# Kernel optimization log

Measured on AMD Instinct MI355X. Metric: run time of the kernel, lower is better.

## Reference

```python
import jax, jax.numpy as jnp
import numpy as np

EPS = 1e-6  # matches module eps


def _l2_norm_ch(t):
    # normalize over channel axis (dim=-2), matching torch l2_norm helper
    return t / jnp.linalg.norm(t, axis=-2, keepdims=True)


def setup_inputs() -> dict:
    key = jax.random.key(0)
    ks = jax.random.split(key, 8)
    B, C, H, W = 8, 256, 128, 128
    m = C // 2  # scale=2
    x = jax.random.normal(ks[0], (B, C, H, W), dtype=jnp.float32)
    Wq = jax.random.normal(ks[1], (m, C), dtype=jnp.float32) * 0.05
    bq = jax.random.normal(ks[2], (m,), dtype=jnp.float32) * 0.05
    Wk = jax.random.normal(ks[3], (m, C), dtype=jnp.float32) * 0.05
    bk = jax.random.normal(ks[4], (m,), dtype=jnp.float32) * 0.05
    Wv = jax.random.normal(ks[5], (C, C), dtype=jnp.float32) * 0.05
    bv = jax.random.normal(ks[6], (C,), dtype=jnp.float32) * 0.05
    # gamma is a zero-init nn.Parameter in the module; use a random scalar so
    # the output is non-trivial for correctness checking.
    gamma = jax.random.normal(ks[7], (1,), dtype=jnp.float32)
    return {"x": x, "Wq": Wq, "bq": bq, "Wk": Wk, "bk": bk, "Wv": Wv, "bv": bv, "gamma": gamma}


def reference(x, Wq, bq, Wk, bk, Wv, bv, gamma):
    B, C, H, W = x.shape  # module names these (batch, channels, width, height)
    N = H * W
    xf = x.reshape(B, C, N)
    # 1x1 convs == per-pixel linear maps over channels
    Q = jnp.einsum('mc,bcn->bmn', Wq, xf) + bq[None, :, None]   # [B, m, N]
    K = jnp.einsum('mc,bcn->bmn', Wk, xf) + bk[None, :, None]   # [B, m, N]
    V = jnp.einsum('oc,bcn->bon', Wv, xf) + bv[None, :, None]   # [B, C, N]
    Qn = _l2_norm_ch(Q).transpose(0, 2, 1)  # [B, N, m]
    Kn = _l2_norm_ch(K)                      # [B, m, N]
    Ksum = jnp.sum(Kn, axis=-1) + EPS        # [B, m]
    tailor = 1.0 / (N + jnp.einsum('bnm,bm->bn', Qn, Ksum))  # [B, N]
    vsum = jnp.sum(V, axis=-1)                                # [B, C]
    matrix = jnp.einsum('bmn,bcn->bmc', Kn, V)                # [B, m, C]
    matrix_sum = vsum[:, :, None] + jnp.einsum('bnm,bmc->bcn', Qn, matrix)  # [B, C, N]
    weight_value = matrix_sum * tailor[:, None, :]
    return (gamma * weight_value).reshape(B, C, H, W)
```

## Files before the change

### kernel.cpp

```cpp
#include <hip/hip_runtime.h>
#include <math.h>

typedef unsigned short ushort_t;
typedef __attribute__((ext_vector_type(4))) float f32x4;
typedef __attribute__((ext_vector_type(8))) short short8;

#define MFMA16(a, b, c) __builtin_amdgcn_mfma_f32_16x16x32_bf16((a), (b), (c), 0, 0, 0)

constexpr int kB = 8;
constexpr int kC = 256;
constexpr int kM = 128;
constexpr int kN = 16384;

constexpr size_t kOffS    = 0;
constexpr size_t kOffKsum = 1048576;
constexpr size_t kOffXsum = 1052672;
constexpr size_t kOffVsum = 1060864;
constexpr size_t kOffWkb  = 1069056;
constexpr size_t kOffWqb  = 1134592;
constexpr size_t kOffMatT = 1200128;

__device__ __forceinline__ ushort_t f2bf(float f) {
  union { float f; unsigned u; } v; v.f = f;
  unsigned r = v.u + 0x7fffu + ((v.u >> 16) & 1u);
  return (ushort_t)(r >> 16);
}
__device__ __forceinline__ float bf2f(ushort_t h) {
  union { float f; unsigned u; } v; v.u = ((unsigned)h) << 16;
  return v.f;
}

__device__ __forceinline__ void sync_lds() {
  __atomic_signal_fence(__ATOMIC_SEQ_CST);
  __builtin_amdgcn_s_waitcnt(0xc07f);
  __builtin_amdgcn_s_barrier();
  __atomic_signal_fence(__ATOMIC_SEQ_CST);
}

__global__ void k0_init(const float* __restrict__ Wq, const float* __restrict__ Wk,
                        float* __restrict__ ws_f, ushort_t* __restrict__ Wkb,
                        ushort_t* __restrict__ Wqb) {
  int i = blockIdx.x * 256 + threadIdx.x;
  for (int j = i; j < 265216; j += 262144) ws_f[j] = 0.0f;
  if (i < kM * kC) {
    Wkb[i] = f2bf(Wk[i]);
    Wqb[i] = f2bf(Wq[i]);
  }
}

__global__ __launch_bounds__(512, 2)
void k1_acc(const float* __restrict__ x, const float* __restrict__ bk,
            const ushort_t* __restrict__ Wkb, float* __restrict__ S,
            float* __restrict__ Ksum, float* __restrict__ xsum) {
  __shared__ __align__(16) ushort_t xb_n[256][40];
  __shared__ __align__(16) ushort_t xb_t[32][264];
  __shared__ __align__(16) ushort_t knb[128][40];
  __shared__ __align__(16) float red[32][12];

  const int t = threadIdx.x;
  const int b = blockIdx.y;
  const int lane = t & 63, w = t >> 6, quad = lane >> 4, l16 = lane & 15;
  const int r8 = t >> 3;
  const int px0 = 4 * (t & 7);

  float bk_r[4];
#pragma unroll
  for (int r = 0; r < 4; ++r) bk_r[r] = bk[16 * w + 4 * quad + r];

  f32x4 accS[16];
#pragma unroll
  for (int ct = 0; ct < 16; ++ct) accS[ct] = (f32x4){0.f, 0.f, 0.f, 0.f};
  float ksump[4] = {0.f, 0.f, 0.f, 0.f};
  float xs_p[4] = {0.f, 0.f, 0.f, 0.f};

  const float* xg = x + ((size_t)(b * kC) + r8) * kN + blockIdx.x * 256 + px0;

  float4 bufA[4], bufB[4];
#pragma unroll
  for (int p = 0; p < 4; ++p)
    bufA[p] = *(const float4*)(xg + (size_t)p * 64 * kN);

  auto step = [&](int ti, float4 (&cur)[4], float4 (&nxt)[4]) {
    sync_lds();
    if (ti < 7) {
#pragma unroll
      for (int p = 0; p < 4; ++p)
        nxt[p] = *(const float4*)(xg + (size_t)p * 64 * kN + (ti + 1) * 32);
    }
#pragma unroll
    for (int p = 0; p < 4; ++p) {
      float4 v = cur[p];
      const int rp = 64 * p + r8;
      xs_p[p] += v.x + v.y + v.z + v.w;
      ushort_t u0 = f2bf(v.x), u1 = f2bf(v.y), u2 = f2bf(v.z), u3 = f2bf(v.w);
      uint2 pk;
      pk.x = (unsigned)u0 | ((unsigned)u1 << 16);
      pk.y = (unsigned)u2 | ((unsigned)u3 << 16);
      *(uint2*)&xb_n[rp][px0] = pk;
      xb_t[px0 + 0][rp] = u0;
      xb_t[px0 + 1][rp] = u1;
      xb_t[px0 + 2][rp] = u2;
      xb_t[px0 + 3][rp] = u3;
    }
    sync_lds();

    f32x4 acc1[2] = {{0.f, 0.f, 0.f, 0.f}, {0.f, 0.f, 0.f, 0.f}};
    const ushort_t* wkbase = Wkb + (16 * w + l16) * 256 + quad * 8;
#pragma unroll
    for (int ks = 0; ks < 8; ++ks) {
      short8 a = *(const short8*)(wkbase + ks * 32);
      short8 b0 = *(const short8*)&xb_t[l16][ks * 32 + quad * 8];
      short8 b1 = *(const short8*)&xb_t[16 + l16][ks * 32 + quad * 8];
      acc1[0] = MFMA16(a, b0, acc1[0]);
      acc1[1] = MFMA16(a, b1, acc1[1]);
    }
    float k0v[4], k1v[4];
    float ssq0 = 0.f, ssq1 = 0.f;
#pragma unroll
    for (int r = 0; r < 4; ++r) {
      k0v[r] = acc1[0][r] + bk_r[r];
      k1v[r] = acc1[1][r] + bk_r[r];
      ssq0 += k0v[r] * k0v[r];
      ssq1 += k1v[r] * k1v[r];
    }
    ssq0 += __shfl_xor(ssq0, 16); ssq0 += __shfl_xor(ssq0, 32);
    ssq1 += __shfl_xor(ssq1, 16); ssq1 += __shfl_xor(ssq1, 32);
    if (quad == 0) { red[l16][w] = ssq0; red[16 + l16][w] = ssq1; }
    sync_lds();

    f32x4 ra = *(const f32x4*)&red[l16][0];
    f32x4 rb = *(const f32x4*)&red[l16][4];
    f32x4 rc = *(const f32x4*)&red[16 + l16][0];
    f32x4 rd = *(const f32x4*)&red[16 + l16][4];
    const float iv0 = rsqrtf(ra[0] + ra[1] + ra[2] + ra[3] + rb[0] + rb[1] + rb[2] + rb[3]);
    const float iv1 = rsqrtf(rc[0] + rc[1] + rc[2] + rc[3] + rd[0] + rd[1] + rd[2] + rd[3]);
#pragma unroll
    for (int r = 0; r < 4; ++r) {
      float kn0 = k0v[r] * iv0, kn1 = k1v[r] * iv1;
      ksump[r] += kn0 + kn1;
      knb[16 * w + 4 * quad + r][l16] = f2bf(kn0);
      knb[16 * w + 4 * quad + r][16 + l16] = f2bf(kn1);
    }
    __builtin_amdgcn_s_waitcnt(0xc07f);

    short8 a2 = *(const short8*)&knb[16 * w + l16][quad * 8];
#pragma unroll
    for (int ct = 0; ct < 16; ++ct) {
      short8 b2 = *(const short8*)&xb_n[ct * 16 + l16][quad * 8];
      accS[ct] = MFMA16(a2, b2, accS[ct]);
    }
  };

  for (int ti = 0; ti < 8; ti += 2) {
    step(ti, bufA, bufB);
    step(ti + 1, bufB, bufA);
  }

  float* Sb = S + (size_t)b * kM * kC;
#pragma unroll
  for (int ct = 0; ct < 16; ++ct)
#pragma unroll
    for (int r = 0; r < 4; ++r)
      atomicAdd(&Sb[(16 * w + 4 * quad + r) * 256 + ct * 16 + l16], accS[ct][r]);
#pragma unroll
  for (int r = 0; r < 4; ++r) {
    float v = ksump[r];
    v += __shfl_xor(v, 1); v += __shfl_xor(v, 2);
    v += __shfl_xor(v, 4); v += __shfl_xor(v, 8);
    if (l16 == 0) atomicAdd(&Ksum[b * kM + 16 * w + 4 * quad + r], v);
  }
#pragma unroll
  for (int p = 0; p < 4; ++p) {
    float v = xs_p[p];
    v += __shfl_xor(v, 1); v += __shfl_xor(v, 2); v += __shfl_xor(v, 4);
    if ((t & 7) == 0) atomicAdd(&xsum[b * kC + 64 * p + r8], v);
  }
}

__global__ __launch_bounds__(256, 4)
void k2_matrix(const float* __restrict__ S, const float* __restrict__ Ksum,
               const float* __restrict__ xsum, const float* __restrict__ Wv,
               const float* __restrict__ bv, ushort_t* __restrict__ matT,
               float* __restrict__ vsum) {
  const int t = threadIdx.x;
  const int lane = t & 63, w = t >> 6, quad = lane >> 4, l16 = lane & 15;
  const int bx = blockIdx.x;
  const int b = bx >> 5, ct = (bx >> 1) & 15, mt = bx & 1;
  const int c0 = ct * 16;
  const int m0 = mt * 64 + w * 16;

  const float* arow = Wv + (size_t)(c0 + l16) * 256 + quad * 8;
  const float* brow = S + ((size_t)b * kM + m0 + l16) * 256 + quad * 8;
  const bool do_vsum = (mt == 0) && (w == 0);
  const float* xsb = xsum + b * kC + quad * 8;

  f32x4 acc = (f32x4){0.f, 0.f, 0.f, 0.f};
  float vdot = 0.f;

#pragma unroll
  for (int ks = 0; ks < 8; ++ks) {
    float4 a0 = *(const float4*)(arow + ks * 32);
    float4 a1 = *(const float4*)(arow + ks * 32 + 4);
    float4 b0 = *(const float4*)(brow + ks * 32);
    float4 b1 = *(const float4*)(brow + ks * 32 + 4);
    float av[8] = {a0.x, a0.y, a0.z, a0.w, a1.x, a1.y, a1.z, a1.w};
    float bw[8] = {b0.x, b0.y, b0.z, b0.w, b1.x, b1.y, b1.z, b1.w};
    if (do_vsum) {
      float4 x0 = *(const float4*)(xsb + ks * 32);
      float4 x1 = *(const float4*)(xsb + ks * 32 + 4);
      vdot += av[0] * x0.x + av[1] * x0.y + av[2] * x0.z + av[3] * x0.w +
              av[4] * x1.x + av[5] * x1.y + av[6] * x1.z + av[7] * x1.w;
    }
    short8 ah, al, bh, bl;
#pragma unroll
    for (int i = 0; i < 8; ++i) {
      ushort_t h = f2bf(av[i]);
      ah[i] = (short)h;
      al[i] = (short)f2bf(av[i] - bf2f(h));
      ushort_t g = f2bf(bw[i]);
      bh[i] = (short)g;
      bl[i] = (short)f2bf(bw[i] - bf2f(g));
    }
    acc = MFMA16(ah, bh, acc);
    acc = MFMA16(ah, bl, acc);
    acc = MFMA16(al, bh, acc);
  }

  const float ksm = Ksum[b * kM + m0 + l16];
  float4 bv4 = *(const float4*)(bv + c0 + quad * 4);
  float bvv[4] = {bv4.x, bv4.y, bv4.z, bv4.w};
#pragma unroll
  for (int r = 0; r < 4; ++r) {
    const int c = c0 + 4 * quad + r;
    matT[((size_t)b * kC + c) * kM + m0 + l16] = f2bf(acc[r] + ksm * bvv[r]);
  }
  if (do_vsum) {
    vdot += __shfl_xor(vdot, 16);
    vdot += __shfl_xor(vdot, 32);
    if (quad == 0)
      vsum[b * kC + c0 + l16] = vdot + 16384.f * bv[c0 + l16];
  }
}

__global__ __launch_bounds__(512, 2)
void k3_out(const float* __restrict__ x, const float* __restrict__ bq,
            const ushort_t* __restrict__ Wqb, const ushort_t* __restrict__ matT,
            const float* __restrict__ Ksum, const float* __restrict__ vsum,
            const float* __restrict__ gamma, float* __restrict__ out) {
  __shared__ __align__(16) ushort_t xb_t[32][264];
  __shared__ __align__(16) ushort_t qnb[32][136];
  __shared__ __align__(16) float red[32][12];
  __shared__ __align__(16) float red2[32][12];

  const int t = threadIdx.x;
  const int b = blockIdx.y;
  const int lane = t & 63, w = t >> 6, quad = lane >> 4, l16 = lane & 15;
  const int r8 = t >> 3;
  const int px0 = 4 * (t & 7);
  const float gm = gamma[0];

  float bq_r[4], ks_r[4], vs_r[2][4];
#pragma unroll
  for (int r = 0; r < 4; ++r) {
    bq_r[r] = bq[16 * w + 4 * quad + r];
    ks_r[r] = Ksum[b * kM + 16 * w + 4 * quad + r] + 1e-6f;
  }
#pragma unroll
  for (int mi = 0; mi < 2; ++mi)
#pragma unroll
    for (int r = 0; r < 4; ++r)
      vs_r[mi][r] = vsum[b * kC + (2 * w + mi) * 16 + 4 * quad + r];

  const float* xg = x + ((size_t)(b * kC) + r8) * kN + blockIdx.x * 256 + px0;

  float4 bufA[4], bufB[4];
#pragma unroll
  for (int p = 0; p < 4; ++p)
    bufA[p] = *(const float4*)(xg + (size_t)p * 64 * kN);

  auto step = [&](int ti, float4 (&cur)[4], float4 (&nxt)[4]) {
    const int n0 = blockIdx.x * 256 + ti * 32;
    sync_lds();
    if (ti < 7) {
#pragma unroll
      for (int p = 0; p < 4; ++p)
        nxt[p] = *(const float4*)(xg + (size_t)p * 64 * kN + (ti + 1) * 32);
    }
#pragma unroll
    for (int p = 0; p < 4; ++p) {
      float4 v = cur[p];
      const int rp = 64 * p + r8;
      xb_t[px0 + 0][rp] = f2bf(v.x);
      xb_t[px0 + 1][rp] = f2bf(v.y);
      xb_t[px0 + 2][rp] = f2bf(v.z);
      xb_t[px0 + 3][rp] = f2bf(v.w);
    }
    sync_lds();

    f32x4 acc1[2] = {{0.f, 0.f, 0.f, 0.f}, {0.f, 0.f, 0.f, 0.f}};
    const ushort_t* wqbase = Wqb + (16 * w + l16) * 256 + quad * 8;
#pragma unroll
    for (int ks = 0; ks < 8; ++ks) {
      short8 a = *(const short8*)(wqbase + ks * 32);
      short8 b0 = *(const short8*)&xb_t[l16][ks * 32 + quad * 8];
      short8 b1 = *(const short8*)&xb_t[16 + l16][ks * 32 + quad * 8];
      acc1[0] = MFMA16(a, b0, acc1[0]);
      acc1[1] = MFMA16(a, b1, acc1[1]);
    }
    float q0v[4], q1v[4];
    float ssq0 = 0.f, ssq1 = 0.f, dot0 = 0.f, dot1 = 0.f;
#pragma unroll
    for (int r = 0; r < 4; ++r) {
      q0v[r] = acc1[0][r] + bq_r[r];
      q1v[r] = acc1[1][r] + bq_r[r];
      ssq0 += q0v[r] * q0v[r]; ssq1 += q1v[r] * q1v[r];
      dot0 += q0v[r] * ks_r[r]; dot1 += q1v[r] * ks_r[r];
    }
    ssq0 += __shfl_xor(ssq0, 16); ssq0 += __shfl_xor(ssq0, 32);
    ssq1 += __shfl_xor(ssq1, 16); ssq1 += __shfl_xor(ssq1, 32);
    dot0 += __shfl_xor(dot0, 16); dot0 += __shfl_xor(dot0, 32);
    dot1 += __shfl_xor(dot1, 16); dot1 += __shfl_xor(dot1, 32);
    if (quad == 0) {
      red[l16][w] = ssq0;  red[16 + l16][w] = ssq1;
      red2[l16][w] = dot0; red2[16 + l16][w] = dot1;
    }
    sync_lds();
    f32x4 ra = *(const f32x4*)&red[l16][0];
    f32x4 rb = *(const f32x4*)&red[l16][4];
    f32x4 rc = *(const f32x4*)&red[16 + l16][0];
    f32x4 rd = *(const f32x4*)&red[16 + l16][4];
    f32x4 da = *(const f32x4*)&red2[l16][0];
    f32x4 db = *(const f32x4*)&red2[l16][4];
    f32x4 dc = *(const f32x4*)&red2[16 + l16][0];
    f32x4 dd = *(const f32x4*)&red2[16 + l16][4];
    const float iv0 = rsqrtf(ra[0] + ra[1] + ra[2] + ra[3] + rb[0] + rb[1] + rb[2] + rb[3]);
    const float iv1 = rsqrtf(rc[0] + rc[1] + rc[2] + rc[3] + rd[0] + rd[1] + rd[2] + rd[3]);
    const float d0 = da[0] + da[1] + da[2] + da[3] + db[0] + db[1] + db[2] + db[3];
    const float d1 = dc[0] + dc[1] + dc[2] + dc[3] + dd[0] + dd[1] + dd[2] + dd[3];
    const float tl0 = 1.f / (16384.f + d0 * iv0);
    const float tl1 = 1.f / (16384.f + d1 * iv1);
    {
      ushort_t q0b[4], q1b[4];
#pragma unroll
      for (int r = 0; r < 4; ++r) {
        q0b[r] = f2bf(q0v[r] * iv0);
        q1b[r] = f2bf(q1v[r] * iv1);
      }
      uint2 p0, p1;
      p0.x = (unsigned)q0b[0] | ((unsigned)q0b[1] << 16);
      p0.y = (unsigned)q0b[2] | ((unsigned)q0b[3] << 16);
      p1.x = (unsigned)q1b[0] | ((unsigned)q1b[1] << 16);
      p1.y = (unsigned)q1b[2] | ((unsigned)q1b[3] << 16);
      *(uint2*)&qnb[l16][16 * w + 4 * quad] = p0;
      *(uint2*)&qnb[16 + l16][16 * w + 4 * quad] = p1;
    }
    sync_lds();

    f32x4 accO[2][2];
#pragma unroll
    for (int mi = 0; mi < 2; ++mi)
#pragma unroll
      for (int nt = 0; nt < 2; ++nt) accO[mi][nt] = (f32x4){0.f, 0.f, 0.f, 0.f};
    const ushort_t* mrow0 = matT + ((size_t)b * kC + (2 * w) * 16 + l16) * kM + quad * 8;
    const ushort_t* mrow1 = mrow0 + 16 * kM;
#pragma unroll
    for (int ks = 0; ks < 4; ++ks) {
      short8 b0 = *(const short8*)&qnb[l16][ks * 32 + quad * 8];
      short8 b1 = *(const short8*)&qnb[16 + l16][ks * 32 + quad * 8];
      short8 a0 = *(const short8*)(mrow0 + ks * 32);
      short8 a1 = *(const short8*)(mrow1 + ks * 32);
      accO[0][0] = MFMA16(a0, b0, accO[0][0]);
      accO[0][1] = MFMA16(a0, b1, accO[0][1]);
      accO[1][0] = MFMA16(a1, b0, accO[1][0]);
      accO[1][1] = MFMA16(a1, b1, accO[1][1]);
    }
#pragma unroll
    for (int mi = 0; mi < 2; ++mi) {
#pragma unroll
      for (int r = 0; r < 4; ++r) {
        const int c = (2 * w + mi) * 16 + 4 * quad + r;
        size_t base = ((size_t)(b * kC + c)) * kN + n0;
        out[base + l16] = gm * tl0 * (vs_r[mi][r] + accO[mi][0][r]);
        out[base + 16 + l16] = gm * tl1 * (vs_r[mi][r] + accO[mi][1][r]);
      }
    }
  };

  for (int ti = 0; ti < 8; ti += 2) {
    step(ti, bufA, bufB);
    step(ti + 1, bufB, bufA);
  }
}

extern "C" void kernel_launch(void* const* d_in, const int* in_sizes, int n_in,
                              void* d_out, int out_size, void* d_ws, size_t ws_size,
                              hipStream_t stream) {
  (void)in_sizes; (void)n_in; (void)out_size; (void)ws_size;
  const float* x     = (const float*)d_in[0];
  const float* Wq    = (const float*)d_in[1];
  const float* bq    = (const float*)d_in[2];
  const float* Wk    = (const float*)d_in[3];
  const float* bk    = (const float*)d_in[4];
  const float* Wv    = (const float*)d_in[5];
  const float* bv    = (const float*)d_in[6];
  const float* gamma = (const float*)d_in[7];
  float* out = (float*)d_out;

  char* wsb = (char*)d_ws;
  float*    S    = (float*)(wsb + kOffS);
  float*    Ksum = (float*)(wsb + kOffKsum);
  float*    xsum = (float*)(wsb + kOffXsum);
  float*    vsum = (float*)(wsb + kOffVsum);
  ushort_t* Wkb  = (ushort_t*)(wsb + kOffWkb);
  ushort_t* Wqb  = (ushort_t*)(wsb + kOffWqb);
  ushort_t* matT = (ushort_t*)(wsb + kOffMatT);

  k0_init<<<1024, 256, 0, stream>>>(Wq, Wk, (float*)wsb, Wkb, Wqb);
  k1_acc<<<dim3(64, 8), 512, 0, stream>>>(x, bk, Wkb, S, Ksum, xsum);
  k2_matrix<<<256, 256, 0, stream>>>(S, Ksum, xsum, Wv, bv, matT, vsum);
  k3_out<<<dim3(64, 8), 512, 0, stream>>>(x, bq, Wqb, matT, Ksum, vsum, gamma, out);
}
```

Baseline: 343.3 us.

## Software-pipeline k1/k3 across tiles, swizzle LDS transposes, raise occupancy

Both k1 and k3 are restructured so each tile's normalization and second GEMM run one iteration behind the first GEMM. Double-buffered LDS reduction and xb_n buffers let this cut the number of barriers per tile from three to two. The transposed bf16 staging buffer gets an XOR swizzle to avoid LDS bank conflicts, padding is removed, and launch bounds rise to 4 blocks per CU. Odd blocks also issue their S atomics in reverse order to reduce contention. Possible costs are register pressure from the higher occupancy target, which could cause spills, and subtle hazards in the hand-placed synchronization.

```diff
diff --git a/kernel.cpp b/kernel.cpp
--- a/kernel.cpp
+++ b/kernel.cpp
@@ -48,20 +48,23 @@
   }
 }
 
-__global__ __launch_bounds__(512, 2)
+__global__ __launch_bounds__(512, 4)
 void k1_acc(const float* __restrict__ x, const float* __restrict__ bk,
             const ushort_t* __restrict__ Wkb, float* __restrict__ S,
             float* __restrict__ Ksum, float* __restrict__ xsum) {
-  __shared__ __align__(16) ushort_t xb_n[256][40];
+  __shared__ __align__(16) ushort_t xb_n[2][256][32];
   __shared__ __align__(16) ushort_t xb_t[32][264];
-  __shared__ __align__(16) ushort_t knb[128][40];
-  __shared__ __align__(16) float red[32][12];
+  __shared__ __align__(16) ushort_t knb[128][32];
+  __shared__ __align__(16) float red[2][32][12];
 
   const int t = threadIdx.x;
   const int b = blockIdx.y;
   const int lane = t & 63, w = t >> 6, quad = lane >> 4, l16 = lane & 15;
   const int r8 = t >> 3;
   const int px0 = 4 * (t & 7);
+  const int xk  = (t & 7) << 3;
+  const int rk0 = (l16 >> 2) << 3;
+  const int rk1 = rk0 ^ 32;
 
   float bk_r[4];
 #pragma unroll
@@ -72,6 +75,7 @@
   for (int ct = 0; ct < 16; ++ct) accS[ct] = (f32x4){0.f, 0.f, 0.f, 0.f};
   float ksump[4] = {0.f, 0.f, 0.f, 0.f};
   float xs_p[4] = {0.f, 0.f, 0.f, 0.f};
+  float k0v[4], k1v[4];
 
   const float* xg = x + ((size_t)(b * kC) + r8) * kN + blockIdx.x * 256 + px0;
 
@@ -80,13 +84,14 @@
   for (int p = 0; p < 4; ++p)
     bufA[p] = *(const float4*)(xg + (size_t)p * 64 * kN);
 
-  auto step = [&](int ti, float4 (&cur)[4], float4 (&nxt)[4]) {
-    sync_lds();
-    if (ti < 7) {
-#pragma unroll
-      for (int p = 0; p < 4; ++p)
-        nxt[p] = *(const float4*)(xg + (size_t)p * 64 * kN + (ti + 1) * 32);
-    }
+  auto prefetch = [&](int ti, float4 (&nxt)[4]) {
+#pragma unroll
+    for (int p = 0; p < 4; ++p)
+      nxt[p] = *(const float4*)(xg + (size_t)p * 64 * kN + ti * 32);
+  };
+
+  auto stage = [&](int ti, float4 (&cur)[4]) {
+    const int tb = ti & 1;
 #pragma unroll
     for (int p = 0; p < 4; ++p) {
       float4 v = cur[p];
@@ -96,25 +101,26 @@
       uint2 pk;
       pk.x = (unsigned)u0 | ((unsigned)u1 << 16);
       pk.y = (unsigned)u2 | ((unsigned)u3 << 16);
-      *(uint2*)&xb_n[rp][px0] = pk;
-      xb_t[px0 + 0][rp] = u0;
-      xb_t[px0 + 1][rp] = u1;
-      xb_t[px0 + 2][rp] = u2;
-      xb_t[px0 + 3][rp] = u3;
-    }
-    sync_lds();
-
+      *(uint2*)&xb_n[tb][rp][px0] = pk;
+      const int cs = rp ^ xk;
+      xb_t[px0 + 0][cs] = u0;
+      xb_t[px0 + 1][cs] = u1;
+      xb_t[px0 + 2][cs] = u2;
+      xb_t[px0 + 3][cs] = u3;
+    }
+  };
+
+  auto gemm1 = [&](int ti) {
     f32x4 acc1[2] = {{0.f, 0.f, 0.f, 0.f}, {0.f, 0.f, 0.f, 0.f}};
     const ushort_t* wkbase = Wkb + (16 * w + l16) * 256 + quad * 8;
 #pragma unroll
     for (int ks = 0; ks < 8; ++ks) {
       short8 a = *(const short8*)(wkbase + ks * 32);
-      short8 b0 = *(const short8*)&xb_t[l16][ks * 32 + quad * 8];
-      short8 b1 = *(const short8*)&xb_t[16 + l16][ks * 32 + quad * 8];
+      short8 b0 = *(const short8*)&xb_t[l16][(ks * 32 + quad * 8) ^ rk0];
+      short8 b1 = *(const short8*)&xb_t[16 + l16][(ks * 32 + quad * 8) ^ rk1];
       acc1[0] = MFMA16(a, b0, acc1[0]);
       acc1[1] = MFMA16(a, b1, acc1[1]);
     }
-    float k0v[4], k1v[4];
     float ssq0 = 0.f, ssq1 = 0.f;
 #pragma unroll
     for (int r = 0; r < 4; ++r) {
@@ -125,13 +131,15 @@
     }
     ssq0 += __shfl_xor(ssq0, 16); ssq0 += __shfl_xor(ssq0, 32);
     ssq1 += __shfl_xor(ssq1, 16); ssq1 += __shfl_xor(ssq1, 32);
-    if (quad == 0) { red[l16][w] = ssq0; red[16 + l16][w] = ssq1; }
-    sync_lds();
-
-    f32x4 ra = *(const f32x4*)&red[l16][0];
-    f32x4 rb = *(const f32x4*)&red[l16][4];
-    f32x4 rc = *(const f32x4*)&red[16 + l16][0];
-    f32x4 rd = *(const f32x4*)&red[16 + l16][4];
+    if (quad == 0) { red[ti & 1][l16][w] = ssq0; red[ti & 1][16 + l16][w] = ssq1; }
+  };
+
+  auto norm_gemm2 = [&](int ti) {
+    const int tb = ti & 1;
+    f32x4 ra = *(const f32x4*)&red[tb][l16][0];
+    f32x4 rb = *(const f32x4*)&red[tb][l16][4];
+    f32x4 rc = *(const f32x4*)&red[tb][16 + l16][0];
+    f32x4 rd = *(const f32x4*)&red[tb][16 + l16][4];
     const float iv0 = rsqrtf(ra[0] + ra[1] + ra[2] + ra[3] + rb[0] + rb[1] + rb[2] + rb[3]);
     const float iv1 = rsqrtf(rc[0] + rc[1] + rc[2] + rc[3] + rd[0] + rd[1] + rd[2] + rd[3]);
 #pragma unroll
@@ -142,26 +150,51 @@
       knb[16 * w + 4 * quad + r][16 + l16] = f2bf(kn1);
     }
     __builtin_amdgcn_s_waitcnt(0xc07f);
-
     short8 a2 = *(const short8*)&knb[16 * w + l16][quad * 8];
 #pragma unroll
     for (int ct = 0; ct < 16; ++ct) {
-      short8 b2 = *(const short8*)&xb_n[ct * 16 + l16][quad * 8];
+      short8 b2 = *(const short8*)&xb_n[tb][ct * 16 + l16][quad * 8];
       accS[ct] = MFMA16(a2, b2, accS[ct]);
     }
   };
 
-  for (int ti = 0; ti < 8; ti += 2) {
-    step(ti, bufA, bufB);
-    step(ti + 1, bufB, bufA);
-  }
+  prefetch(1, bufB);
+  stage(0, bufA);
+  sync_lds();
+  gemm1(0);
+
+  auto iter = [&](int ti, float4 (&cur)[4], float4 (&nxt)[4], bool pf) {
+    sync_lds();
+    if (pf) prefetch(ti + 1, nxt);
+    norm_gemm2(ti - 1);
+    stage(ti, cur);
+    sync_lds();
+    gemm1(ti);
+  };
+  iter(1, bufB, bufA, true);
+  iter(2, bufA, bufB, true);
+  iter(3, bufB, bufA, true);
+  iter(4, bufA, bufB, true);
+  iter(5, bufB, bufA, true);
+  iter(6, bufA, bufB, true);
+  iter(7, bufB, bufA, false);
+  sync_lds();
+  norm_gemm2(7);
 
   float* Sb = S + (size_t)b * kM * kC;
-#pragma unroll
-  for (int ct = 0; ct < 16; ++ct)
-#pragma unroll
-    for (int r = 0; r < 4; ++r)
-      atomicAdd(&Sb[(16 * w + 4 * quad + r) * 256 + ct * 16 + l16], accS[ct][r]);
+  if ((blockIdx.x & 1) == 0) {
+#pragma unroll
+    for (int ct = 0; ct < 16; ++ct)
+#pragma unroll
+      for (int r = 0; r < 4; ++r)
+        atomicAdd(&Sb[(16 * w + 4 * quad + r) * 256 + ct * 16 + l16], accS[ct][r]);
+  } else {
+#pragma unroll
+    for (int ct = 15; ct >= 0; --ct)
+#pragma unroll
+      for (int r = 0; r < 4; ++r)
+        atomicAdd(&Sb[(16 * w + 4 * quad + r) * 256 + ct * 16 + l16], accS[ct][r]);
+  }
 #pragma unroll
   for (int r = 0; r < 4; ++r) {
     float v = ksump[r];
@@ -242,21 +275,24 @@
   }
 }
 
-__global__ __launch_bounds__(512, 2)
+__global__ __launch_bounds__(512, 4)
 void k3_out(const float* __restrict__ x, const float* __restrict__ bq,
             const ushort_t* __restrict__ Wqb, const ushort_t* __restrict__ matT,
             const float* __restrict__ Ksum, const float* __restrict__ vsum,
             const float* __restrict__ gamma, float* __restrict__ out) {
   __shared__ __align__(16) ushort_t xb_t[32][264];
   __shared__ __align__(16) ushort_t qnb[32][136];
-  __shared__ __align__(16) float red[32][12];
-  __shared__ __align__(16) float red2[32][12];
+  __shared__ __align__(16) float red[2][32][12];
+  __shared__ __align__(16) float red2[2][32][12];
 
   const int t = threadIdx.x;
   const int b = blockIdx.y;
   const int lane = t & 63, w = t >> 6, quad = lane >> 4, l16 = lane & 15;
   const int r8 = t >> 3;
   const int px0 = 4 * (t & 7);
+  const int xk  = (t & 7) << 3;
+  const int rk0 = (l16 >> 2) << 3;
+  const int rk1 = rk0 ^ 32;
   const float gm = gamma[0];
 
   float bq_r[4], ks_r[4], vs_r[2][4];
@@ -271,6 +307,9 @@
     for (int r = 0; r < 4; ++r)
       vs_r[mi][r] = vsum[b * kC + (2 * w + mi) * 16 + 4 * quad + r];
 
+  float q0v[4], q1v[4];
+  float tl0, tl1;
+
   const float* xg = x + ((size_t)(b * kC) + r8) * kN + blockIdx.x * 256 + px0;
 
   float4 bufA[4], bufB[4];
@@ -278,36 +317,35 @@
   for (int p = 0; p < 4; ++p)
     bufA[p] = *(const float4*)(xg + (size_t)p * 64 * kN);
 
-  auto step = [&](int ti, float4 (&cur)[4], float4 (&nxt)[4]) {
-    const int n0 = blockIdx.x * 256 + ti * 32;
-    sync_lds();
-    if (ti < 7) {
-#pragma unroll
-      for (int p = 0; p < 4; ++p)
-        nxt[p] = *(const float4*)(xg + (size_t)p * 64 * kN + (ti + 1) * 32);
-    }
+  auto prefetch3 = [&](int ti, float4 (&nxt)[4]) {
+#pragma unroll
+    for (int p = 0; p < 4; ++p)
+      nxt[p] = *(const float4*)(xg + (size_t)p * 64 * kN + ti * 32);
+  };
+
+  auto stage3 = [&](float4 (&cur)[4]) {
 #pragma unroll
     for (int p = 0; p < 4; ++p) {
       float4 v = cur[p];
-      const int rp = 64 * p + r8;
-      xb_t[px0 + 0][rp] = f2bf(v.x);
-      xb_t[px0 + 1][rp] = f2bf(v.y);
-      xb_t[px0 + 2][rp] = f2bf(v.z);
-      xb_t[px0 + 3][rp] = f2bf(v.w);
-    }
-    sync_lds();
-
+      const int cs = (64 * p + r8) ^ xk;
+      xb_t[px0 + 0][cs] = f2bf(v.x);
+      xb_t[px0 + 1][cs] = f2bf(v.y);
+      xb_t[px0 + 2][cs] = f2bf(v.z);
+      xb_t[px0 + 3][cs] = f2bf(v.w);
+    }
+  };
+
+  auto qproj = [&](int ti) {
     f32x4 acc1[2] = {{0.f, 0.f, 0.f, 0.f}, {0.f, 0.f, 0.f, 0.f}};
     const ushort_t* wqbase = Wqb + (16 * w + l16) * 256 + quad * 8;
 #pragma unroll
     for (int ks = 0; ks < 8; ++ks) {
       short8 a = *(const short8*)(wqbase + ks * 32);
-      short8 b0 = *(const short8*)&xb_t[l16][ks * 32 + quad * 8];
-      short8 b1 = *(const short8*)&xb_t[16 + l16][ks * 32 + quad * 8];
+      short8 b0 = *(const short8*)&xb_t[l16][(ks * 32 + quad * 8) ^ rk0];
+      short8 b1 = *(const short8*)&xb_t[16 + l16][(ks * 32 + quad * 8) ^ rk1];
       acc1[0] = MFMA16(a, b0, acc1[0]);
       acc1[1] = MFMA16(a, b1, acc1[1]);
     }
-    float q0v[4], q1v[4];
     float ssq0 = 0.f, ssq1 = 0.f, dot0 = 0.f, dot1 = 0.f;
 #pragma unroll
     for (int r = 0; r < 4; ++r) {
@@ -321,41 +359,44 @@
     dot0 += __shfl_xor(dot0, 16); dot0 += __shfl_xor(dot0, 32);
     dot1 += __shfl_xor(dot1, 16); dot1 += __shfl_xor(dot1, 32);
     if (quad == 0) {
-      red[l16][w] = ssq0;  red[16 + l16][w] = ssq1;
-      red2[l16][w] = dot0; red2[16 + l16][w] = dot1;
-    }
-    sync_lds();
-    f32x4 ra = *(const f32x4*)&red[l16][0];
-    f32x4 rb = *(const f32x4*)&red[l16][4];
-    f32x4 rc = *(const f32x4*)&red[16 + l16][0];
-    f32x4 rd = *(const f32x4*)&red[16 + l16][4];
-    f32x4 da = *(const f32x4*)&red2[l16][0];
-    f32x4 db = *(const f32x4*)&red2[l16][4];
-    f32x4 dc = *(const f32x4*)&red2[16 + l16][0];
-    f32x4 dd = *(const f32x4*)&red2[16 + l16][4];
+      red[ti & 1][l16][w] = ssq0;  red[ti & 1][16 + l16][w] = ssq1;
+      red2[ti & 1][l16][w] = dot0; red2[ti & 1][16 + l16][w] = dot1;
+    }
+  };
+
+  auto normq = [&](int ti) {
+    const int tb = ti & 1;
+    f32x4 ra = *(const f32x4*)&red[tb][l16][0];
+    f32x4 rb = *(const f32x4*)&red[tb][l16][4];
+    f32x4 rc = *(const f32x4*)&red[tb][16 + l16][0];
+    f32x4 rd = *(const f32x4*)&red[tb][16 + l16][4];
+    f32x4 da = *(const f32x4*)&red2[tb][l16][0];
+    f32x4 db = *(const f32x4*)&red2[tb][l16][4];
+    f32x4 dc = *(const f32x4*)&red2[tb][16 + l16][0];
+    f32x4 dd = *(const f32x4*)&red2[tb][16 + l16][4];
     const float iv0 = rsqrtf(ra[0] + ra[1] + ra[2] + ra[3] + rb[0] + rb[1] + rb[2] + rb[3]);
     const float iv1 = rsqrtf(rc[0] + rc[1] + rc[2] + rc[3] + rd[0] + rd[1] + rd[2] + rd[3]);
     const float d0 = da[0] + da[1] + da[2] + da[3] + db[0] + db[1] + db[2] + db[3];
     const float d1 = dc[0] + dc[1] + dc[2] + dc[3] + dd[0] + dd[1] + dd[2] + dd[3];
-    const float tl0 = 1.f / (16384.f + d0 * iv0);
-    const float tl1 = 1.f / (16384.f + d1 * iv1);
-    {
-      ushort_t q0b[4], q1b[4];
-#pragma unroll
-      for (int r = 0; r < 4; ++r) {
-        q0b[r] = f2bf(q0v[r] * iv0);
-        q1b[r] = f2bf(q1v[r] * iv1);
-      }
-      uint2 p0, p1;
-      p0.x = (unsigned)q0b[0] | ((unsigned)q0b[1] << 16);
-      p0.y = (unsigned)q0b[2] | ((unsigned)q0b[3] << 16);
-      p1.x = (unsigned)q1b[0] | ((unsigned)q1b[1] << 16);
-      p1.y = (unsigned)q1b[2] | ((unsigned)q1b[3] << 16);
-      *(uint2*)&qnb[l16][16 * w + 4 * quad] = p0;
-      *(uint2*)&qnb[16 + l16][16 * w + 4 * quad] = p1;
-    }
-    sync_lds();
-
+    tl0 = 1.f / (16384.f + d0 * iv0);
+    tl1 = 1.f / (16384.f + d1 * iv1);
+    ushort_t q0b[4], q1b[4];
+#pragma unroll
+    for (int r = 0; r < 4; ++r) {
+      q0b[r] = f2bf(q0v[r] * iv0);
+      q1b[r] = f2bf(q1v[r] * iv1);
+    }
+    uint2 p0, p1;
+    p0.x = (unsigned)q0b[0] | ((unsigned)q0b[1] << 16);
+    p0.y = (unsigned)q0b[2] | ((unsigned)q0b[3] << 16);
+    p1.x = (unsigned)q1b[0] | ((unsigned)q1b[1] << 16);
+    p1.y = (unsigned)q1b[2] | ((unsigned)q1b[3] << 16);
+    *(uint2*)&qnb[l16][16 * w + 4 * quad] = p0;
+    *(uint2*)&qnb[16 + l16][16 * w + 4 * quad] = p1;
+  };
+
+  auto outg = [&](int ti) {
+    const int n0 = blockIdx.x * 256 + ti * 32;
     f32x4 accO[2][2];
 #pragma unroll
     for (int mi = 0; mi < 2; ++mi)
@@ -386,10 +427,31 @@
     }
   };
 
-  for (int ti = 0; ti < 8; ti += 2) {
-    step(ti, bufA, bufB);
-    step(ti + 1, bufB, bufA);
-  }
+  prefetch3(1, bufB);
+  stage3(bufA);
+  sync_lds();
+  qproj(0);
+
+  auto iter3 = [&](int ti, float4 (&cur)[4], float4 (&nxt)[4], bool pf) {
+    sync_lds();
+    if (pf) prefetch3(ti + 1, nxt);
+    normq(ti - 1);
+    stage3(cur);
+    sync_lds();
+    qproj(ti);
+    outg(ti - 1);
+  };
+  iter3(1, bufB, bufA, true);
+  iter3(2, bufA, bufB, true);
+  iter3(3, bufB, bufA, true);
+  iter3(4, bufA, bufB, true);
+  iter3(5, bufB, bufA, true);
+  iter3(6, bufA, bufB, true);
+  iter3(7, bufB, bufA, false);
+  sync_lds();
+  normq(7);
+  sync_lds();
+  outg(7);
 }
 
 extern "C" void kernel_launch(void* const* d_in, const int* in_sizes, int n_in,
```

Result: slower. 508.2 us (+48.0%).

## Spread S atomics over 16 partial buffers with reduce kernel; XOR-swizzle transposed LDS tile

Applied to the files above, without the earlier changes.

Each k1 block now atomically adds its S tile into one of 16 partial buffers per batch, chosen by blockIdx.x. Half the blocks walk the column tiles in reverse order, and a new reduce kernel sums the partials into S. This is meant to cut atomic contention, since 64 blocks per batch all used to add into the same S. In exchange it zeroes and reads an extra 16 MB of workspace and adds a kernel launch. Separately, the transposed bf16 x tile drops its row padding and uses an XOR swizzle instead, aiming to reduce LDS bank conflicts in both k1 and k3.

```diff
diff --git a/kernel.cpp b/kernel.cpp
--- a/kernel.cpp
+++ b/kernel.cpp
@@ -12,13 +12,14 @@
 constexpr int kM = 128;
 constexpr int kN = 16384;
 
-constexpr size_t kOffS    = 0;
-constexpr size_t kOffKsum = 1048576;
-constexpr size_t kOffXsum = 1052672;
-constexpr size_t kOffVsum = 1060864;
-constexpr size_t kOffWkb  = 1069056;
-constexpr size_t kOffWqb  = 1134592;
-constexpr size_t kOffMatT = 1200128;
+constexpr size_t kOffSp   = 0;
+constexpr size_t kOffS    = 16777216;
+constexpr size_t kOffKsum = 17825792;
+constexpr size_t kOffXsum = 17829888;
+constexpr size_t kOffVsum = 17838080;
+constexpr size_t kOffWkb  = 17846272;
+constexpr size_t kOffWqb  = 17911808;
+constexpr size_t kOffMatT = 17977344;
 
 __device__ __forceinline__ ushort_t f2bf(float f) {
   union { float f; unsigned u; } v; v.f = f;
@@ -41,7 +42,11 @@
                         float* __restrict__ ws_f, ushort_t* __restrict__ Wkb,
                         ushort_t* __restrict__ Wqb) {
   int i = blockIdx.x * 256 + threadIdx.x;
-  for (int j = i; j < 265216; j += 262144) ws_f[j] = 0.0f;
+  float4 z = {0.f, 0.f, 0.f, 0.f};
+  float4* sp4 = (float4*)ws_f;
+#pragma unroll
+  for (int j = 0; j < 4; ++j) sp4[i + j * 262144] = z;
+  if (i < 3072) ws_f[4456448 + i] = 0.0f;
   if (i < kM * kC) {
     Wkb[i] = f2bf(Wk[i]);
     Wqb[i] = f2bf(Wq[i]);
@@ -50,10 +55,10 @@
 
 __global__ __launch_bounds__(512, 2)
 void k1_acc(const float* __restrict__ x, const float* __restrict__ bk,
-            const ushort_t* __restrict__ Wkb, float* __restrict__ S,
+            const ushort_t* __restrict__ Wkb, float* __restrict__ Sp,
             float* __restrict__ Ksum, float* __restrict__ xsum) {
   __shared__ __align__(16) ushort_t xb_n[256][40];
-  __shared__ __align__(16) ushort_t xb_t[32][264];
+  __shared__ __align__(16) ushort_t xb_t[32][256];
   __shared__ __align__(16) ushort_t knb[128][40];
   __shared__ __align__(16) float red[32][12];
 
@@ -62,6 +67,9 @@
   const int lane = t & 63, w = t >> 6, quad = lane >> 4, l16 = lane & 15;
   const int r8 = t >> 3;
   const int px0 = 4 * (t & 7);
+  const int key01 = (((px0 >> 1)) & 7) << 3;
+  const int key23 = key01 ^ 8;
+  const int rk = ((l16 >> 1) & 7) << 3;
 
   float bk_r[4];
 #pragma unroll
@@ -97,10 +105,10 @@
       pk.x = (unsigned)u0 | ((unsigned)u1 << 16);
       pk.y = (unsigned)u2 | ((unsigned)u3 << 16);
       *(uint2*)&xb_n[rp][px0] = pk;
-      xb_t[px0 + 0][rp] = u0;
-      xb_t[px0 + 1][rp] = u1;
-      xb_t[px0 + 2][rp] = u2;
-      xb_t[px0 + 3][rp] = u3;
+      xb_t[px0 + 0][rp ^ key01] = u0;
+      xb_t[px0 + 1][rp ^ key01] = u1;
+      xb_t[px0 + 2][rp ^ key23] = u2;
+      xb_t[px0 + 3][rp ^ key23] = u3;
     }
     sync_lds();
 
@@ -109,8 +117,8 @@
 #pragma unroll
     for (int ks = 0; ks < 8; ++ks) {
       short8 a = *(const short8*)(wkbase + ks * 32);
-      short8 b0 = *(const short8*)&xb_t[l16][ks * 32 + quad * 8];
-      short8 b1 = *(const short8*)&xb_t[16 + l16][ks * 32 + quad * 8];
+      short8 b0 = *(const short8*)&xb_t[l16][(ks * 32 + quad * 8) ^ rk];
+      short8 b1 = *(const short8*)&xb_t[16 + l16][(ks * 32 + quad * 8) ^ rk];
       acc1[0] = MFMA16(a, b0, acc1[0]);
       acc1[1] = MFMA16(a, b1, acc1[1]);
     }
@@ -156,12 +164,20 @@
     step(ti + 1, bufB, bufA);
   }
 
-  float* Sb = S + (size_t)b * kM * kC;
-#pragma unroll
-  for (int ct = 0; ct < 16; ++ct)
-#pragma unroll
-    for (int r = 0; r < 4; ++r)
-      atomicAdd(&Sb[(16 * w + 4 * quad + r) * 256 + ct * 16 + l16], accS[ct][r]);
+  float* Sb = Sp + ((size_t)(b * 16) + (blockIdx.x & 15)) * kM * kC;
+  if (((blockIdx.x >> 4) & 1) == 0) {
+#pragma unroll
+    for (int ct = 0; ct < 16; ++ct)
+#pragma unroll
+      for (int r = 0; r < 4; ++r)
+        atomicAdd(&Sb[(16 * w + 4 * quad + r) * 256 + ct * 16 + l16], accS[ct][r]);
+  } else {
+#pragma unroll
+    for (int ct = 15; ct >= 0; --ct)
+#pragma unroll
+      for (int r = 0; r < 4; ++r)
+        atomicAdd(&Sb[(16 * w + 4 * quad + r) * 256 + ct * 16 + l16], accS[ct][r]);
+  }
 #pragma unroll
   for (int r = 0; r < 4; ++r) {
     float v = ksump[r];
@@ -175,6 +191,17 @@
     v += __shfl_xor(v, 1); v += __shfl_xor(v, 2); v += __shfl_xor(v, 4);
     if ((t & 7) == 0) atomicAdd(&xsum[b * kC + 64 * p + r8], v);
   }
+}
+
+__global__ __launch_bounds__(256)
+void k1_reduce(const float* __restrict__ Sp, float* __restrict__ S) {
+  const int idx = blockIdx.x * 256 + threadIdx.x;
+  const int b = idx >> 15, rem = idx & 32767;
+  const float* base = Sp + (((size_t)b * 16) << 15) + rem;
+  float s = 0.f;
+#pragma unroll
+  for (int p = 0; p < 16; ++p) s += base[(size_t)p << 15];
+  S[idx] = s;
 }
 
 __global__ __launch_bounds__(256, 4)
@@ -247,7 +274,7 @@
             const ushort_t* __restrict__ Wqb, const ushort_t* __restrict__ matT,
             const float* __restrict__ Ksum, const float* __restrict__ vsum,
             const float* __restrict__ gamma, float* __restrict__ out) {
-  __shared__ __align__(16) ushort_t xb_t[32][264];
+  __shared__ __align__(16) ushort_t xb_t[32][256];
   __shared__ __align__(16) ushort_t qnb[32][136];
   __shared__ __align__(16) float red[32][12];
   __shared__ __align__(16) float red2[32][12];
@@ -257,6 +284,9 @@
   const int lane = t & 63, w = t >> 6, quad = lane >> 4, l16 = lane & 15;
   const int r8 = t >> 3;
   const int px0 = 4 * (t & 7);
+  const int key01 = (((px0 >> 1)) & 7) << 3;
+  const int key23 = key01 ^ 8;
+  const int rk = ((l16 >> 1) & 7) << 3;
   const float gm = gamma[0];
 
   float bq_r[4], ks_r[4], vs_r[2][4];
@@ -290,10 +320,10 @@
     for (int p = 0; p < 4; ++p) {
       float4 v = cur[p];
       const int rp = 64 * p + r8;
-      xb_t[px0 + 0][rp] = f2bf(v.x);
-      xb_t[px0 + 1][rp] = f2bf(v.y);
-      xb_t[px0 + 2][rp] = f2bf(v.z);
-      xb_t[px0 + 3][rp] = f2bf(v.w);
+      xb_t[px0 + 0][rp ^ key01] = f2bf(v.x);
+      xb_t[px0 + 1][rp ^ key01] = f2bf(v.y);
+      xb_t[px0 + 2][rp ^ key23] = f2bf(v.z);
+      xb_t[px0 + 3][rp ^ key23] = f2bf(v.w);
     }
     sync_lds();
 
@@ -302,8 +332,8 @@
 #pragma unroll
     for (int ks = 0; ks < 8; ++ks) {
       short8 a = *(const short8*)(wqbase + ks * 32);
-      short8 b0 = *(const short8*)&xb_t[l16][ks * 32 + quad * 8];
-      short8 b1 = *(const short8*)&xb_t[16 + l16][ks * 32 + quad * 8];
+      short8 b0 = *(const short8*)&xb_t[l16][(ks * 32 + quad * 8) ^ rk];
+      short8 b1 = *(const short8*)&xb_t[16 + l16][(ks * 32 + quad * 8) ^ rk];
       acc1[0] = MFMA16(a, b0, acc1[0]);
       acc1[1] = MFMA16(a, b1, acc1[1]);
     }
@@ -407,6 +437,7 @@
   float* out = (float*)d_out;
 
   char* wsb = (char*)d_ws;
+  float*    Sp   = (float*)(wsb + kOffSp);
   float*    S    = (float*)(wsb + kOffS);
   float*    Ksum = (float*)(wsb + kOffKsum);
   float*    xsum = (float*)(wsb + kOffXsum);
@@ -416,7 +447,8 @@
   ushort_t* matT = (ushort_t*)(wsb + kOffMatT);
 
   k0_init<<<1024, 256, 0, stream>>>(Wq, Wk, (float*)wsb, Wkb, Wqb);
-  k1_acc<<<dim3(64, 8), 512, 0, stream>>>(x, bk, Wkb, S, Ksum, xsum);
+  k1_acc<<<dim3(64, 8), 512, 0, stream>>>(x, bk, Wkb, Sp, Ksum, xsum);
+  k1_reduce<<<1024, 256, 0, stream>>>(Sp, S);
   k2_matrix<<<256, 256, 0, stream>>>(S, Ksum, xsum, Wv, bv, matT, vsum);
   k3_out<<<dim3(64, 8), 512, 0, stream>>>(x, bq, Wqb, matT, Ksum, vsum, gamma, out);
 }
```

New measurement: 343.3 us. No clear change (-0.0%).
